# Optimization experiments

Hardware: AMD Instinct MI355X
Metric: run time of the kernel (lower is better)

Reference implementation:

```python
import jax, jax.numpy as jnp
import numpy as np

DN = ('NCHW', 'OIHW', 'NCHW')

def conv3x3(x, w):
    return jax.lax.conv_general_dilated(x, w, (1, 1), [(1, 1), (1, 1)], dimension_numbers=DN)

def setup_inputs() -> dict:
    key = jax.random.key(0)
    ks = jax.random.split(key, 5)
    N, C, H, W = 64, 512, 16, 16
    fan = C * 3 * 3
    s = 1.0 / np.sqrt(fan)
    x = jax.random.normal(ks[0], (N, C, H, W), dtype=jnp.float32)
    Wq = jax.random.normal(ks[1], (C, C, 3, 3), dtype=jnp.float32) * s
    Wk = jax.random.normal(ks[2], (C, C, 3, 3), dtype=jnp.float32) * s
    Wv = jax.random.normal(ks[3], (C, C, 3, 3), dtype=jnp.float32) * s
    Wc = jax.random.normal(ks[4], (C, C, 3, 3), dtype=jnp.float32) * s
    gamma = jnp.ones((C,), dtype=jnp.float32)
    beta = jnp.zeros((C,), dtype=jnp.float32)
    return {"x": x, "Wq": Wq, "Wk": Wk, "Wv": Wv, "Wc": Wc, "gamma": gamma, "beta": beta}

def reference(x, Wq, Wk, Wv, Wc, gamma, beta):
    C = x.shape[1]
    q = conv3x3(x, Wq)  # [N,C,H,W]
    k = conv3x3(x, Wk)
    v = conv3x3(x, Wv)
    # att[n,m,h,w] = sum_c q[n,c,h,w] * k[m,c,h,w] / sqrt(C); softmax over m
    att = jnp.einsum('nchw,mchw->nmhw', q, k) / jnp.sqrt(jnp.float32(C))
    att = jax.nn.softmax(att, axis=1)
    # virt[n,c,h,w] = sum_m att[n,m,h,w] * v[m,c,h,w]
    virt = jnp.einsum('nmhw,mchw->nchw', att, v)
    # GroupNorm(1, C): normalize over (C,H,W) per sample, per-channel affine
    mu = jnp.mean(virt, axis=(1, 2, 3), keepdims=True)
    var = jnp.var(virt, axis=(1, 2, 3), keepdims=True)
    virt = (virt - mu) * jax.lax.rsqrt(var + 1e-5)
    virt = virt * gamma[None, :, None, None] + beta[None, :, None, None]
    virt = jax.nn.relu(virt)
    virt = conv3x3(virt, Wc)
    # Dropout is identity in eval mode
    return x + virt
```

## Files before the change

kernel.cpp:

```cpp
#include <hip/hip_runtime.h>
#include <math.h>

typedef unsigned short u16;
typedef unsigned int u32;
typedef short short8 __attribute__((ext_vector_type(8)));
typedef float f32x4 __attribute__((ext_vector_type(4)));

#define NB 64
#define CCH 512
#define HW 256

__device__ __forceinline__ u16 f2bf(float f) {
    union { float f; u32 u; } x; x.f = f;
    u32 r = x.u + 0x7fffu + ((x.u >> 16) & 1u);
    return (u16)(r >> 16);
}
__device__ __forceinline__ float bf2f(u16 b) {
    union { u32 u; float f; } x; x.u = ((u32)b) << 16;
    return x.f;
}
__device__ __forceinline__ void gload_lds16(const u16* g, u16* l) {
    __builtin_amdgcn_global_load_lds((const __attribute__((address_space(1))) u32*)g,
                                     (__attribute__((address_space(3))) u32*)l, 16, 0, 0);
}

__global__ __launch_bounds__(256) void zero_borders(u16* __restrict__ pad) {
    const int n = blockIdx.x, t = threadIdx.x;
    short8 z = (short8){0,0,0,0,0,0,0,0};
    for (int idx = t; idx < 68 * 64; idx += 256) {
        int cell = idx >> 6, ch = idx & 63;
        int hh, ww;
        if (cell < 18)      { hh = 0;          ww = cell; }
        else if (cell < 36) { hh = 17;         ww = cell - 18; }
        else if (cell < 52) { hh = cell - 35;  ww = 0; }
        else                { hh = cell - 51;  ww = 17; }
        *(short8*)(pad + ((size_t)((n * 18 + hh) * 18 + ww)) * 512 + ch * 8) = z;
    }
}

__global__ __launch_bounds__(256) void prep_x(const float* __restrict__ x, u16* __restrict__ pad) {
    __shared__ float tl[64][65];
    const int n = blockIdx.z, c0 = blockIdx.y * 64, p0 = blockIdx.x * 64;
    const int t = threadIdx.x;
    {
        const int cc = t >> 2, ps = (t & 3) * 16;
#pragma unroll
        for (int i = 0; i < 4; ++i) {
            float4 v4 = *(const float4*)(x + (((size_t)(n * 512 + c0 + cc)) << 8) + p0 + ps + i * 4);
            tl[cc][ps + i * 4 + 0] = v4.x;
            tl[cc][ps + i * 4 + 1] = v4.y;
            tl[cc][ps + i * 4 + 2] = v4.z;
            tl[cc][ps + i * 4 + 3] = v4.w;
        }
    }
    __syncthreads();
    {
        const int pp = t >> 2, cs = (t & 3) * 16;
        short8 o0, o1;
#pragma unroll
        for (int i = 0; i < 8; ++i) o0[i] = (short)f2bf(tl[cs + i][pp]);
#pragma unroll
        for (int i = 0; i < 8; ++i) o1[i] = (short)f2bf(tl[cs + 8 + i][pp]);
        const int p = p0 + pp, h = p >> 4, wcol = p & 15;
        u16* dst = pad + ((size_t)((n * 18 + h + 1) * 18 + wcol + 1)) * 512 + c0 + cs;
        *(short8*)(dst + 0) = o0;
        *(short8*)(dst + 8) = o1;
    }
}

__global__ __launch_bounds__(256) void prep_w(
    const float* __restrict__ Wq, const float* __restrict__ Wk,
    const float* __restrict__ Wv, const float* __restrict__ Wc,
    u16* __restrict__ Wt)
{
    __shared__ float lw[4608];
    const int co = blockIdx.x, sel = blockIdx.y, t = threadIdx.x;
    const float* Ws = (sel == 0) ? Wq : (sel == 1) ? Wk : (sel == 2) ? Wv : Wc;
#pragma unroll
    for (int i = 0; i < 18; ++i) lw[t + i * 256] = Ws[(size_t)co * 4608 + t + i * 256];
    __syncthreads();
    for (int tap = 0; tap < 9; ++tap)
#pragma unroll
        for (int hh = 0; hh < 2; ++hh) {
            int ci = t + hh * 256;
            Wt[(((size_t)(sel * 9 + tap)) << 18) + (co << 9) + ci] = f2bf(lw[ci * 9 + tap]);
        }
}

__global__ __launch_bounds__(512, 1) void qkv_mfma8(
    const u16* __restrict__ pad, const u16* __restrict__ Wt,
    u16* __restrict__ q, u16* __restrict__ k, u16* __restrict__ v)
{
    __shared__ short As[4][8192];
    __shared__ short Bs[4][6144];
    const int t = threadIdx.x;
    const int l = t & 63;
    const int wid = t >> 6;
    const int wm = wid >> 2, wn = wid & 3;

    const int o = blockIdx.x;
    const int wg = (o & 7) * 64 + (o >> 3);
    const int imbase = (wg >> 3) * 256;
    const int cobase = (wg & 7) * 192;

    const int cl = ((l & 3) - ((l >> 3) & 3)) & 3;
    int imoffA[2], woffB[2];
#pragma unroll
    for (int rr = 0; rr < 2; ++rr) {
        const int chunk = wid * 2 + rr;
        const int imrow = imbase + chunk * 16 + (l >> 2);
        const int p = imrow >> 6, n = imrow & 63;
        imoffA[rr] = ((n * 18 + (p >> 4)) * 18 + (p & 15)) * 512 + cl * 8;
        const int cof = cobase + chunk * 16 + (l >> 2);
        const int sel = cof >> 9, co = cof & 511;
        woffB[rr] = sel * 9 * 262144 + co * 512 + cl * 8;
    }

    const int fp = ((l >> 4) + (l >> 1)) & 3;
    const int aoff = (wm * 128 + (l & 15)) * 32 + fp * 8;
    const int boff = (wn * 48 + (l & 15)) * 32 + fp * 8;

    f32x4 acc[8][3];
#pragma unroll
    for (int i = 0; i < 8; ++i)
#pragma unroll
        for (int j = 0; j < 3; ++j) acc[i][j] = (f32x4){0.f, 0.f, 0.f, 0.f};

    auto STAGE_A = [&](int kt, int s) {
        const int tap = kt >> 4;
        const int shift = ((tap / 3) * 18 + (tap % 3)) * 512 + (kt & 15) * 32;
#pragma unroll
        for (int rr = 0; rr < 2; ++rr)
            gload_lds16(pad + imoffA[rr] + shift, (u16*)(&As[s][0] + (wid * 2 + rr) * 512));
    };
    auto STAGE_B = [&](int kt, int s) {
        if (wid < 6) {
            const int tap = kt >> 4;
            const int shift = tap * 262144 + (kt & 15) * 32;
#pragma unroll
            for (int rr = 0; rr < 2; ++rr)
                gload_lds16(Wt + woffB[rr] + shift, (u16*)(&Bs[s][0] + (wid * 2 + rr) * 512));
        }
    };

    STAGE_A(0, 0); STAGE_B(0, 0);
    STAGE_A(1, 1); STAGE_B(1, 1);
    STAGE_A(2, 2); STAGE_B(2, 2);
    if (wid < 6) asm volatile("s_waitcnt vmcnt(8)" ::: "memory");
    else         asm volatile("s_waitcnt vmcnt(4)" ::: "memory");
    __builtin_amdgcn_sched_barrier(0);
    __builtin_amdgcn_s_barrier();
    __builtin_amdgcn_sched_barrier(0);

    short8 A0[8], A1[8], B0[3], B1[3];
#pragma unroll
    for (int j = 0; j < 3; ++j) B0[j] = *(const short8*)(&Bs[0][0] + boff + j * 512);
#pragma unroll
    for (int i = 0; i < 8; ++i) A0[i] = *(const short8*)(&As[0][0] + aoff + i * 512);

#define QSTEP(KT, BUFR, BUFS, AM, BMF, AR, BRF)                                   \
    {                                                                             \
        if ((KT) >= 142)  asm volatile("s_waitcnt vmcnt(0)" ::: "memory");        \
        else if (wid < 6) asm volatile("s_waitcnt vmcnt(4)" ::: "memory");        \
        else              asm volatile("s_waitcnt vmcnt(2)" ::: "memory");        \
        __builtin_amdgcn_sched_barrier(0);                                        \
        __builtin_amdgcn_s_barrier();                                             \
        __builtin_amdgcn_sched_barrier(0);                                        \
        if ((KT) < 143) {                                                         \
            const short* Abr = &As[BUFR][0];                                      \
            const short* Bbr = &Bs[BUFR][0];                                      \
            _Pragma("unroll")                                                     \
            for (int j = 0; j < 3; ++j) BRF[j] = *(const short8*)(Bbr + boff + j * 512); \
            _Pragma("unroll")                                                     \
            for (int i = 0; i < 8; ++i) AR[i] = *(const short8*)(Abr + aoff + i * 512);  \
        }                                                                         \
        if ((KT) + 3 < 144) { STAGE_A((KT) + 3, BUFS); STAGE_B((KT) + 3, BUFS); } \
        __builtin_amdgcn_s_setprio(1);                                            \
        _Pragma("unroll")                                                         \
        for (int i = 0; i < 8; ++i)                                               \
            _Pragma("unroll")                                                     \
            for (int j = 0; j < 3; ++j)                                           \
                acc[i][j] = __builtin_amdgcn_mfma_f32_16x16x32_bf16(AM[i], BMF[j], acc[i][j], 0, 0, 0); \
        __builtin_amdgcn_s_setprio(0);                                            \
    }

#pragma unroll 1
    for (int kt = 0; kt < 144; kt += 4) {
        QSTEP(kt + 0, 1, 3, A0, B0, A1, B1);
        QSTEP(kt + 1, 2, 0, A1, B1, A0, B0);
        QSTEP(kt + 2, 3, 1, A0, B0, A1, B1);
        QSTEP(kt + 3, 0, 2, A1, B1, A0, B0);
    }
#undef QSTEP

#pragma unroll
    for (int j = 0; j < 3; ++j) {
        const int colb = cobase + wn * 48 + j * 16;
        u16* op = ((colb >> 9) == 0) ? q : (((colb >> 9) == 1) ? k : v);
        op += (colb & 511) + (l & 15);
#pragma unroll
        for (int i = 0; i < 8; ++i) {
            const int row = imbase + wm * 128 + i * 16 + (l >> 4) * 4;
#pragma unroll
            for (int r = 0; r < 4; ++r)
                op[(size_t)(row + r) * 512] = f2bf(acc[i][j][r]);
        }
    }
}

__global__ __launch_bounds__(512, 1) void cres_pipe(
    const u16* __restrict__ pad, const u16* __restrict__ WtC,
    const float* __restrict__ xres, float* __restrict__ out)
{
    __shared__ short As[4][4096];
    __shared__ short Bs[4][8192];
    const int t = threadIdx.x;
    const int l = t & 63;
    const int wid = t >> 6;
    const int wm = wid >> 2, wn = wid & 3;

    const int cobase = (blockIdx.x & 3) * 128;
    const int imbase = (blockIdx.x >> 2) * 256;

    const int cl = ((l & 3) - ((l >> 3) & 3)) & 3;
    int woffA, imoffB[2];
    {
        const int co = cobase + wid * 16 + (l >> 2);
        woffA = co * 512 + cl * 8;
    }
#pragma unroll
    for (int rr = 0; rr < 2; ++rr) {
        const int u = wid * 2 + rr;
        const int imrow = imbase + u * 16 + (l >> 2);
        const int n = imrow >> 8, p = imrow & 255;
        imoffB[rr] = ((n * 18 + (p >> 4)) * 18 + (p & 15)) * 512 + cl * 8;
    }

    const int fp = ((l >> 4) + (l >> 1)) & 3;
    const int aoff = (wm * 64 + (l & 15)) * 32 + fp * 8;
    const int boff = (wn * 64 + (l & 15)) * 32 + fp * 8;

    f32x4 acc[4][4];
#pragma unroll
    for (int i = 0; i < 4; ++i)
#pragma unroll
        for (int j = 0; j < 4; ++j) acc[i][j] = (f32x4){0.f, 0.f, 0.f, 0.f};

    auto STAGE_CA = [&](int kt, int s) {
        const int tap = kt >> 4;
        const int shift = tap * 262144 + (kt & 15) * 32;
        gload_lds16(WtC + woffA + shift, (u16*)(&As[s][0] + wid * 512));
    };
    auto STAGE_CB = [&](int kt, int s) {
        const int tap = kt >> 4;
        const int shift = ((tap / 3) * 18 + (tap % 3)) * 512 + (kt & 15) * 32;
#pragma unroll
        for (int rr = 0; rr < 2; ++rr)
            gload_lds16(pad + imoffB[rr] + shift, (u16*)(&Bs[s][0] + (wid * 2 + rr) * 512));
    };

    STAGE_CA(0, 0); STAGE_CB(0, 0);
    STAGE_CA(1, 1); STAGE_CB(1, 1);
    STAGE_CA(2, 2); STAGE_CB(2, 2);
    asm volatile("s_waitcnt vmcnt(6)" ::: "memory");
    __builtin_amdgcn_sched_barrier(0);
    __builtin_amdgcn_s_barrier();
    __builtin_amdgcn_sched_barrier(0);

    short8 A0[4], A1[4], B0[4], B1[4];
#pragma unroll
    for (int i = 0; i < 4; ++i) A0[i] = *(const short8*)(&As[0][0] + aoff + i * 512);
#pragma unroll
    for (int j = 0; j < 4; ++j) B0[j] = *(const short8*)(&Bs[0][0] + boff + j * 512);

#define CSTEP(KT, BUFR, BUFS, AM, BMF, AR, BRF)                                   \
    {                                                                             \
        if ((KT) >= 142) asm volatile("s_waitcnt vmcnt(0)" ::: "memory");         \
        else             asm volatile("s_waitcnt vmcnt(3)" ::: "memory");         \
        __builtin_amdgcn_sched_barrier(0);                                        \
        __builtin_amdgcn_s_barrier();                                             \
        __builtin_amdgcn_sched_barrier(0);                                        \
        if ((KT) < 143) {                                                         \
            const short* Abr = &As[BUFR][0];                                      \
            const short* Bbr = &Bs[BUFR][0];                                      \
            _Pragma("unroll")                                                     \
            for (int i = 0; i < 4; ++i) AR[i] = *(const short8*)(Abr + aoff + i * 512);  \
            _Pragma("unroll")                                                     \
            for (int j = 0; j < 4; ++j) BRF[j] = *(const short8*)(Bbr + boff + j * 512); \
        }                                                                         \
        if ((KT) + 3 < 144) { STAGE_CA((KT) + 3, BUFS); STAGE_CB((KT) + 3, BUFS); } \
        __builtin_amdgcn_s_setprio(1);                                            \
        _Pragma("unroll")                                                         \
        for (int i = 0; i < 4; ++i)                                               \
            _Pragma("unroll")                                                     \
            for (int j = 0; j < 4; ++j)                                           \
                acc[i][j] = __builtin_amdgcn_mfma_f32_16x16x32_bf16(AM[i], BMF[j], acc[i][j], 0, 0, 0); \
        __builtin_amdgcn_s_setprio(0);                                            \
    }

#pragma unroll 1
    for (int kt = 0; kt < 144; kt += 4) {
        CSTEP(kt + 0, 1, 3, A0, B0, A1, B1);
        CSTEP(kt + 1, 2, 0, A1, B1, A0, B0);
        CSTEP(kt + 2, 3, 1, A0, B0, A1, B1);
        CSTEP(kt + 3, 0, 2, A1, B1, A0, B0);
    }
#undef CSTEP

#pragma unroll
    for (int i = 0; i < 4; ++i)
#pragma unroll
        for (int j = 0; j < 4; ++j)
#pragma unroll
            for (int r = 0; r < 4; ++r) {
                int co = cobase + wm * 64 + i * 16 + (l >> 4) * 4 + r;
                int imrow = imbase + wn * 64 + j * 16 + (l & 15);
                int n = imrow >> 8, p = imrow & 255;
                size_t addr = (((size_t)(n * 512 + co)) << 8) + p;
                out[addr] = acc[i][j][r] + xres[addr];
            }
}

__global__ __launch_bounds__(256) void attn_kernel(
    const u16* __restrict__ qT, const u16* __restrict__ kT, u16* vvT)
{
    const int p = blockIdx.x;
    const int t = threadIdx.x;
    __shared__ float smemA[2][64][68];
    __shared__ float attb[64][68];
    const size_t pb = (size_t)p * (NB * CCH);

    const int ng = t >> 4, mg = t & 15;
    const int n0 = ng * 4, m0 = mg * 4;
    float acc[4][4];
#pragma unroll
    for (int i = 0; i < 4; ++i)
#pragma unroll
        for (int j = 0; j < 4; ++j) acc[i][j] = 0.f;

    for (int ct = 0; ct < 8; ++ct) {
        const int c0 = ct * 64;
        __syncthreads();
#pragma unroll
        for (int s = 0; s < 2; ++s) {
            int f = t + s * 256;
            int nn = f >> 3, c8 = (f & 7) * 8;
            short8 qv = *(const short8*)(qT + pb + (size_t)nn * CCH + c0 + c8);
            short8 kv = *(const short8*)(kT + pb + (size_t)nn * CCH + c0 + c8);
#pragma unroll
            for (int e = 0; e < 8; ++e) {
                smemA[0][nn][c8 + e] = bf2f((u16)qv[e]);
                smemA[1][nn][c8 + e] = bf2f((u16)kv[e]);
            }
        }
        __syncthreads();
#pragma unroll 4
        for (int c4 = 0; c4 < 16; ++c4) {
            float4 q4[4], k4[4];
#pragma unroll
            for (int i = 0; i < 4; ++i) q4[i] = *(const float4*)&smemA[0][n0 + i][c4 * 4];
#pragma unroll
            for (int j = 0; j < 4; ++j) k4[j] = *(const float4*)&smemA[1][m0 + j][c4 * 4];
#pragma unroll
            for (int i = 0; i < 4; ++i)
#pragma unroll
                for (int j = 0; j < 4; ++j) {
                    acc[i][j] = fmaf(q4[i].x, k4[j].x, acc[i][j]);
                    acc[i][j] = fmaf(q4[i].y, k4[j].y, acc[i][j]);
                    acc[i][j] = fmaf(q4[i].z, k4[j].z, acc[i][j]);
                    acc[i][j] = fmaf(q4[i].w, k4[j].w, acc[i][j]);
                }
        }
    }

    const float SCALE = 0.0441941738241592f;
#pragma unroll
    for (int i = 0; i < 4; ++i) {
        float m = fmaxf(fmaxf(acc[i][0], acc[i][1]), fmaxf(acc[i][2], acc[i][3]));
#pragma unroll
        for (int mask = 1; mask < 16; mask <<= 1) m = fmaxf(m, __shfl_xor(m, mask, 16));
        float e[4]; float s = 0.f;
#pragma unroll
        for (int j = 0; j < 4; ++j) { e[j] = __expf((acc[i][j] - m) * SCALE); s += e[j]; }
#pragma unroll
        for (int mask = 1; mask < 16; mask <<= 1) s += __shfl_xor(s, mask, 16);
        float inv = 1.f / s;
#pragma unroll
        for (int j = 0; j < 4; ++j) attb[n0 + i][m0 + j] = e[j] * inv;
    }
    __syncthreads();

    float* vs = &smemA[0][0][0];
    const int ng2 = t >> 3, cg = t & 7;
    const int nn0 = ng2 * 2, cb = cg * 16;
    for (int ct4 = 0; ct4 < 4; ++ct4) {
        const int c0 = ct4 * 128;
#pragma unroll
        for (int s = 0; s < 4; ++s) {
            int f = t + s * 256;
            int m = f >> 4, c8 = (f & 15) * 8;
            short8 vv = *(const short8*)(vvT + pb + (size_t)m * CCH + c0 + c8);
#pragma unroll
            for (int e = 0; e < 8; ++e) vs[m * 132 + c8 + e] = bf2f((u16)vv[e]);
        }
        __syncthreads();
        float acc2[2][16];
#pragma unroll
        for (int i = 0; i < 2; ++i)
#pragma unroll
            for (int j = 0; j < 16; ++j) acc2[i][j] = 0.f;
#pragma unroll 4
        for (int m = 0; m < 64; ++m) {
            float a0 = attb[nn0][m], a1 = attb[nn0 + 1][m];
#pragma unroll
            for (int k4 = 0; k4 < 4; ++k4) {
                float4 v4 = *(const float4*)&vs[m * 132 + cb + k4 * 4];
                acc2[0][k4 * 4 + 0] = fmaf(a0, v4.x, acc2[0][k4 * 4 + 0]);
                acc2[0][k4 * 4 + 1] = fmaf(a0, v4.y, acc2[0][k4 * 4 + 1]);
                acc2[0][k4 * 4 + 2] = fmaf(a0, v4.z, acc2[0][k4 * 4 + 2]);
                acc2[0][k4 * 4 + 3] = fmaf(a0, v4.w, acc2[0][k4 * 4 + 3]);
                acc2[1][k4 * 4 + 0] = fmaf(a1, v4.x, acc2[1][k4 * 4 + 0]);
                acc2[1][k4 * 4 + 1] = fmaf(a1, v4.y, acc2[1][k4 * 4 + 1]);
                acc2[1][k4 * 4 + 2] = fmaf(a1, v4.z, acc2[1][k4 * 4 + 2]);
                acc2[1][k4 * 4 + 3] = fmaf(a1, v4.w, acc2[1][k4 * 4 + 3]);
            }
        }
#pragma unroll
        for (int i = 0; i < 2; ++i)
#pragma unroll
            for (int j = 0; j < 16; ++j)
                vvT[pb + (size_t)(nn0 + i) * CCH + c0 + cb + j] = f2bf(acc2[i][j]);
        __syncthreads();
    }
}

__global__ __launch_bounds__(256) void gn_part1(
    const u16* __restrict__ virtT, float* __restrict__ partials)
{
    const int n = blockIdx.x >> 2, qr = blockIdx.x & 3, t = threadIdx.x;
    float sum = 0.f, ss = 0.f;
#pragma unroll 4
    for (int it = 0; it < 16; ++it) {
        int f = t + it * 256;
        int p = qr * 64 + (f >> 6), c = (f & 63) * 8;
        short8 vv = *(const short8*)(virtT + ((size_t)(p * 64 + n)) * 512 + c);
#pragma unroll
        for (int e = 0; e < 8; ++e) { float x = bf2f((u16)vv[e]); sum += x; ss = fmaf(x, x, ss); }
    }
#pragma unroll
    for (int off = 32; off > 0; off >>= 1) {
        sum += __shfl_down(sum, off);
        ss  += __shfl_down(ss, off);
    }
    __shared__ float rs[4], rss[4];
    const int wid = t >> 6, lane = t & 63;
    if (lane == 0) { rs[wid] = sum; rss[wid] = ss; }
    __syncthreads();
    if (t == 0) {
        partials[(n * 4 + qr) * 2 + 0] = rs[0] + rs[1] + rs[2] + rs[3];
        partials[(n * 4 + qr) * 2 + 1] = rss[0] + rss[1] + rss[2] + rss[3];
    }
}

__global__ __launch_bounds__(256) void gn_part2(
    const u16* __restrict__ virtT, const float* __restrict__ partials,
    const float* __restrict__ gamma, const float* __restrict__ beta,
    u16* __restrict__ ypad)
{
    const int n = blockIdx.x >> 2, qr = blockIdx.x & 3, t = threadIdx.x;
    __shared__ float sg[512], sb[512];
    for (int i = t; i < 512; i += 256) { sg[i] = gamma[i]; sb[i] = beta[i]; }
    float S = 0.f, SS = 0.f;
#pragma unroll
    for (int i = 0; i < 4; ++i) {
        S  += partials[(n * 4 + i) * 2 + 0];
        SS += partials[(n * 4 + i) * 2 + 1];
    }
    const float mu = S * (1.f / 131072.f);
    const float var = SS * (1.f / 131072.f) - mu * mu;
    const float rstd = rsqrtf(var + 1e-5f);
    __syncthreads();

#pragma unroll 4
    for (int it = 0; it < 16; ++it) {
        int f = t + it * 256;
        int p = qr * 64 + (f >> 6), cc = (f & 63) * 8;
        short8 vv = *(const short8*)(virtT + ((size_t)(p * 64 + n)) * 512 + cc);
        short8 ov;
#pragma unroll
        for (int e = 0; e < 8; ++e) {
            float x = (bf2f((u16)vv[e]) - mu) * rstd;
            x = fmaf(x, sg[cc + e], sb[cc + e]);
            ov[e] = (short)f2bf(fmaxf(x, 0.f));
        }
        int h = p >> 4, wcol = p & 15;
        *(short8*)(ypad + ((size_t)((n * 18 + h + 1) * 18 + wcol + 1)) * 512 + cc) = ov;
    }
}

extern "C" void kernel_launch(void* const* d_in, const int* in_sizes, int n_in,
                              void* d_out, int out_size, void* d_ws, size_t ws_size,
                              hipStream_t stream)
{
    const float* x     = (const float*)d_in[0];
    const float* Wq    = (const float*)d_in[1];
    const float* Wk    = (const float*)d_in[2];
    const float* Wv    = (const float*)d_in[3];
    const float* Wc    = (const float*)d_in[4];
    const float* gamma = (const float*)d_in[5];
    const float* beta  = (const float*)d_in[6];
    float* out = (float*)d_out;

    u16* pad = (u16*)d_ws;
    u16* Wt  = pad + 10616832;
    u16* q   = Wt + 9437184;
    u16* k   = q + 8388608;
    u16* v   = k + 8388608;
    float* gnp = (float*)k;

    zero_borders<<<dim3(64), dim3(256), 0, stream>>>(pad);
    prep_x<<<dim3(4, 8, 64), dim3(256), 0, stream>>>(x, pad);
    prep_w<<<dim3(512, 4), dim3(256), 0, stream>>>(Wq, Wk, Wv, Wc, Wt);

    qkv_mfma8<<<dim3(512), dim3(512), 0, stream>>>(pad, Wt, q, k, v);
    attn_kernel<<<dim3(256), dim3(256), 0, stream>>>(q, k, v);
    gn_part1<<<dim3(256), dim3(256), 0, stream>>>(v, gnp);
    gn_part2<<<dim3(256), dim3(256), 0, stream>>>(v, gnp, gamma, beta, pad);
    cres_pipe<<<dim3(256), dim3(512), 0, stream>>>(pad, Wt + 3 * 2359296, x, out);
}
```

Baseline: 399.0 us.

## Restructure QKV conv GEMM pipeline to 3-stage buffering with split half-tile MFMA phases

```diff
diff --git a/kernel.cpp b/kernel.cpp
--- a/kernel.cpp
+++ b/kernel.cpp
@@ -91,8 +91,8 @@
     const u16* __restrict__ pad, const u16* __restrict__ Wt,
     u16* __restrict__ q, u16* __restrict__ k, u16* __restrict__ v)
 {
-    __shared__ short As[4][8192];
-    __shared__ short Bs[4][6144];
+    __shared__ short As[3][8192];
+    __shared__ short Bs[3][6144];
     const int t = threadIdx.x;
     const int l = t & 63;
     const int wid = t >> 6;
@@ -145,53 +145,66 @@
 
     STAGE_A(0, 0); STAGE_B(0, 0);
     STAGE_A(1, 1); STAGE_B(1, 1);
-    STAGE_A(2, 2); STAGE_B(2, 2);
-    if (wid < 6) asm volatile("s_waitcnt vmcnt(8)" ::: "memory");
-    else         asm volatile("s_waitcnt vmcnt(4)" ::: "memory");
+    if (wid < 6) asm volatile("s_waitcnt vmcnt(4)" ::: "memory");
+    else         asm volatile("s_waitcnt vmcnt(2)" ::: "memory");
     __builtin_amdgcn_sched_barrier(0);
     __builtin_amdgcn_s_barrier();
     __builtin_amdgcn_sched_barrier(0);
 
-    short8 A0[8], A1[8], B0[3], B1[3];
-#pragma unroll
-    for (int j = 0; j < 3; ++j) B0[j] = *(const short8*)(&Bs[0][0] + boff + j * 512);
-#pragma unroll
-    for (int i = 0; i < 8; ++i) A0[i] = *(const short8*)(&As[0][0] + aoff + i * 512);
-
-#define QSTEP(KT, BUFR, BUFS, AM, BMF, AR, BRF)                                   \
-    {                                                                             \
-        if ((KT) >= 142)  asm volatile("s_waitcnt vmcnt(0)" ::: "memory");        \
-        else if (wid < 6) asm volatile("s_waitcnt vmcnt(4)" ::: "memory");        \
-        else              asm volatile("s_waitcnt vmcnt(2)" ::: "memory");        \
-        __builtin_amdgcn_sched_barrier(0);                                        \
-        __builtin_amdgcn_s_barrier();                                             \
-        __builtin_amdgcn_sched_barrier(0);                                        \
-        if ((KT) < 143) {                                                         \
-            const short* Abr = &As[BUFR][0];                                      \
-            const short* Bbr = &Bs[BUFR][0];                                      \
-            _Pragma("unroll")                                                     \
-            for (int j = 0; j < 3; ++j) BRF[j] = *(const short8*)(Bbr + boff + j * 512); \
-            _Pragma("unroll")                                                     \
-            for (int i = 0; i < 8; ++i) AR[i] = *(const short8*)(Abr + aoff + i * 512);  \
-        }                                                                         \
-        if ((KT) + 3 < 144) { STAGE_A((KT) + 3, BUFS); STAGE_B((KT) + 3, BUFS); } \
-        __builtin_amdgcn_s_setprio(1);                                            \
-        _Pragma("unroll")                                                         \
-        for (int i = 0; i < 8; ++i)                                               \
-            _Pragma("unroll")                                                     \
-            for (int j = 0; j < 3; ++j)                                           \
-                acc[i][j] = __builtin_amdgcn_mfma_f32_16x16x32_bf16(AM[i], BMF[j], acc[i][j], 0, 0, 0); \
-        __builtin_amdgcn_s_setprio(0);                                            \
-    }
-
+    int s0 = 0;
+    short8 fa[4], fa2[4], fb[3];
 #pragma unroll 1
-    for (int kt = 0; kt < 144; kt += 4) {
-        QSTEP(kt + 0, 1, 3, A0, B0, A1, B1);
-        QSTEP(kt + 1, 2, 0, A1, B1, A0, B0);
-        QSTEP(kt + 2, 3, 1, A0, B0, A1, B1);
-        QSTEP(kt + 3, 0, 2, A1, B1, A0, B0);
-    }
-#undef QSTEP
+    for (int kt = 0; kt < 144; ++kt) {
+        const int s2 = (s0 == 0) ? 2 : s0 - 1;
+        const short* Ab = &As[s0][0];
+        const short* Bb = &Bs[s0][0];
+
+#pragma unroll
+        for (int j = 0; j < 3; ++j) fb[j] = *(const short8*)(Bb + boff + j * 512);
+#pragma unroll
+        for (int i = 0; i < 4; ++i) fa[i] = *(const short8*)(Ab + aoff + i * 512);
+        if (kt < 142) STAGE_A(kt + 2, s2);
+        __builtin_amdgcn_sched_barrier(0);
+        __builtin_amdgcn_s_barrier();
+        asm volatile("s_waitcnt lgkmcnt(0)" ::: "memory");
+        __builtin_amdgcn_sched_barrier(0);
+        __builtin_amdgcn_s_setprio(1);
+#pragma unroll
+        for (int i = 0; i < 4; ++i)
+#pragma unroll
+            for (int j = 0; j < 3; ++j)
+                acc[i][j] = __builtin_amdgcn_mfma_f32_16x16x32_bf16(fa[i], fb[j], acc[i][j], 0, 0, 0);
+        __builtin_amdgcn_s_setprio(0);
+        __builtin_amdgcn_sched_barrier(0);
+        __builtin_amdgcn_s_barrier();
+
+#pragma unroll
+        for (int i = 0; i < 4; ++i) fa2[i] = *(const short8*)(Ab + aoff + 2048 + i * 512);
+        if (kt < 142) STAGE_B(kt + 2, s2);
+        __builtin_amdgcn_sched_barrier(0);
+        __builtin_amdgcn_s_barrier();
+        asm volatile("s_waitcnt lgkmcnt(0)" ::: "memory");
+        __builtin_amdgcn_sched_barrier(0);
+        __builtin_amdgcn_s_setprio(1);
+#pragma unroll
+        for (int i = 0; i < 4; ++i)
+#pragma unroll
+            for (int j = 0; j < 3; ++j)
+                acc[4 + i][j] = __builtin_amdgcn_mfma_f32_16x16x32_bf16(fa2[i], fb[j], acc[4 + i][j], 0, 0, 0);
+        __builtin_amdgcn_s_setprio(0);
+        if (kt >= 142) {
+            asm volatile("s_waitcnt vmcnt(0)" ::: "memory");
+        } else if (wid < 6) {
+            asm volatile("s_waitcnt vmcnt(4)" ::: "memory");
+        } else {
+            asm volatile("s_waitcnt vmcnt(2)" ::: "memory");
+        }
+        __builtin_amdgcn_sched_barrier(0);
+        __builtin_amdgcn_s_barrier();
+        __builtin_amdgcn_sched_barrier(0);
+
+        s0 = (s0 == 2) ? 0 : s0 + 1;
+    }
 
 #pragma unroll
     for (int j = 0; j < 3; ++j) {
```

Result: slower. 420.9 us (+5.5%).
